# Performance work log

Hardware: AMD Instinct MI355X
Metric: run time of the kernel (lower is better)

## Reference

```python
import jax, jax.numpy as jnp
import numpy as np

N = 50000  # nodes


def gcn_layer(x, src, dst, W, b):
    """DGL GraphConv with norm='both': D_in^{-1/2} A^T D_out^{-1/2} x W + b."""
    E = src.shape[0]
    ones = jnp.ones((E,), dtype=x.dtype)
    deg_out = jax.ops.segment_sum(ones, src, num_segments=N)  # out-degree of src nodes
    deg_in = jax.ops.segment_sum(ones, dst, num_segments=N)   # in-degree of dst nodes
    norm_src = jax.lax.rsqrt(jnp.maximum(deg_out, 1.0))
    norm_dst = jax.lax.rsqrt(jnp.maximum(deg_in, 1.0))
    h = x * norm_src[:, None]
    agg = jax.ops.segment_sum(h[src], dst, num_segments=N)  # [N, in_dim]
    return (agg @ W) * norm_dst[:, None] + b


def encoder(feat, src, dst, W1, b1, W2, b2):
    h = jax.nn.relu(gcn_layer(feat, src, dst, W1, b1))
    h = jax.nn.relu(gcn_layer(h, src, dst, W2, b2))
    return h


def proj(h, fc1_W, fc1_b, fc2_W, fc2_b):
    z = jax.nn.elu(h @ fc1_W + fc1_b)
    return z @ fc2_W + fc2_b


def setup_inputs() -> dict:
    key = jax.random.key(0)
    ks = jax.random.split(key, 12)
    in_dim, hid, out_dim, E = 128, 128, 128, 800000
    inp = {
        "feat1": jax.random.normal(ks[0], (N, in_dim), dtype=jnp.float32),
        "feat2": jax.random.normal(ks[1], (N, in_dim), dtype=jnp.float32),
        "edge_index1": jax.random.randint(ks[2], (2, E), 0, N),
        "edge_index2": jax.random.randint(ks[3], (2, E), 0, N),
        # GraphConv weights: in_dim -> 2*hid -> hid
        "conv1_W": jax.random.normal(ks[4], (in_dim, 2 * hid), dtype=jnp.float32) * 0.05,
        "conv1_b": jnp.zeros((2 * hid,), dtype=jnp.float32),
        "conv2_W": jax.random.normal(ks[5], (2 * hid, hid), dtype=jnp.float32) * 0.05,
        "conv2_b": jnp.zeros((hid,), dtype=jnp.float32),
        # MLP proj: fc1 hid->out, fc2 out->hid
        "fc1_W": jax.random.normal(ks[6], (hid, out_dim), dtype=jnp.float32) * 0.05,
        "fc1_b": jnp.zeros((out_dim,), dtype=jnp.float32),
        "fc2_W": jax.random.normal(ks[7], (out_dim, hid), dtype=jnp.float32) * 0.05,
        "fc2_b": jnp.zeros((hid,), dtype=jnp.float32),
    }
    return inp


def reference(feat1, feat2, edge_index1, edge_index2,
              conv1_W, conv1_b, conv2_W, conv2_b,
              fc1_W, fc1_b, fc2_W, fc2_b):
    h1 = encoder(feat1, edge_index1[0], edge_index1[1], conv1_W, conv1_b, conv2_W, conv2_b)
    h2 = encoder(feat2, edge_index2[0], edge_index2[1], conv1_W, conv1_b, conv2_W, conv2_b)
    z1 = proj(h1, fc1_W, fc1_b, fc2_W, fc2_b)
    z2 = proj(h2, fc1_W, fc1_b, fc2_W, fc2_b)
    return (z1, z2)
```

## Files before the change

### kernel.cpp

```cpp
#include <hip/hip_runtime.h>
#include <math.h>

#define NDIM 128
#define H2   256
#define MAXG 2
#define TPE  8192
#define NBKMAX 512

typedef __attribute__((ext_vector_type(8))) short bf16x8;
typedef __attribute__((ext_vector_type(4))) float f32x4;

__device__ __forceinline__ unsigned short f2bf(float f) {
    unsigned int u = __float_as_uint(f);
    u += 0x7fffu + ((u >> 16) & 1u);
    return (unsigned short)(u >> 16);
}
__device__ __forceinline__ float bf2f(unsigned short h) {
    return __uint_as_float(((unsigned int)h) << 16);
}
__device__ __forceinline__ void split2(float f, unsigned short& h, unsigned short& l) {
    h = f2bf(f);
    l = f2bf(f - bf2f(h));
}

struct BinArgs {
    const int* src[MAXG]; const int* dst[MAXG];
    int* histD[MAXG]; int* histS[MAXG];
    int* totD[MAXG];  int* baseD[MAXG];
    int* totS[MAXG];  int* baseS[MAXG];
    unsigned int* pairs[MAXG];
    unsigned short* srcS[MAXG];
    int E[MAXG]; int NBK; int NT; int n;
};

__global__ __launch_bounds__(256) void binA(BinArgs a) {
    __shared__ int cntD[NBKMAX], cntS[NBKMAX];
    int g = blockIdx.y, t = blockIdx.x, tid = threadIdx.x;
    for (int b = tid; b < NBKMAX; b += 256) { cntD[b] = 0; cntS[b] = 0; }
    __syncthreads();
    int E = a.E[g];
    int base = t * TPE;
#pragma unroll
    for (int k = 0; k < TPE / 256; ++k) {
        int e = base + k * 256 + tid;
        if (e < E) {
            atomicAdd(&cntD[a.dst[g][e] >> 7], 1);
            atomicAdd(&cntS[a.src[g][e] >> 7], 1);
        }
    }
    __syncthreads();
    for (int b = tid; b < a.NBK; b += 256) {
        a.histD[g][t * a.NBK + b] = cntD[b];
        a.histS[g][t * a.NBK + b] = cntS[b];
    }
}

__global__ __launch_bounds__(512) void binB(BinArgs a) {
    int g = blockIdx.y, side = blockIdx.z;
    int* hist = side ? a.histS[g] : a.histD[g];
    int* tot  = side ? a.totS[g]  : a.totD[g];
    int* base = side ? a.baseS[g] : a.baseD[g];
    __shared__ int s[512];
    int b = threadIdx.x;
    int v = 0;
    if (b < a.NBK)
        for (int t = 0; t < a.NT; ++t) v += hist[t * a.NBK + b];
    s[b] = v;
    __syncthreads();
    for (int off = 1; off < 512; off <<= 1) {
        int u = (b >= off) ? s[b - off] : 0;
        __syncthreads();
        s[b] += u;
        __syncthreads();
    }
    int excl = s[b] - v;
    if (b < a.NBK) {
        tot[b] = v;
        base[b] = excl;
        int run = excl;
        for (int t = 0; t < a.NT; ++t) {
            int h = hist[t * a.NBK + b];
            hist[t * a.NBK + b] = run;
            run += h;
        }
    }
}

__global__ __launch_bounds__(256) void binC(BinArgs a) {
    __shared__ int offD[NBKMAX], offS[NBKMAX];
    int g = blockIdx.y, t = blockIdx.x, tid = threadIdx.x;
    for (int b = tid; b < a.NBK; b += 256) {
        offD[b] = a.histD[g][t * a.NBK + b];
        offS[b] = a.histS[g][t * a.NBK + b];
    }
    __syncthreads();
    int E = a.E[g];
    int base = t * TPE;
    unsigned int* pairs = a.pairs[g];
    unsigned short* ss = a.srcS[g];
#pragma unroll
    for (int k = 0; k < TPE / 256; ++k) {
        int e = base + k * 256 + tid;
        if (e < E) {
            int s = a.src[g][e], d = a.dst[g][e];
            int pos = atomicAdd(&offD[d >> 7], 1);
            pairs[pos] = ((unsigned int)(d & 127) << 16) | (unsigned int)s;
            int posS = atomicAdd(&offS[s >> 7], 1);
            ss[posS] = (unsigned short)s;
        }
    }
}

struct FinArgs {
    const unsigned int* pairs[MAXG];
    const unsigned short* srcS[MAXG];
    const int* totD[MAXG]; const int* baseD[MAXG];
    const int* totS[MAXG]; const int* baseS[MAXG];
    int* row_ptr[MAXG]; int* row_end[MAXG];
    unsigned short* edge_srt[MAXG];
    float* ns[MAXG]; float* nd[MAXG];
    int n;
};

__global__ __launch_bounds__(256) void finalize(FinArgs a) {
    __shared__ int cnt[128], hist[128], scn[128], cur[128];
    int g = blockIdx.y, bkt = blockIdx.x, tid = threadIdx.x;
    if (tid < 128) { cnt[tid] = 0; hist[tid] = 0; }
    __syncthreads();
    {
        int base = a.baseS[g][bkt], tot = a.totS[g][bkt];
        const unsigned short* ss = a.srcS[g];
        for (int i = tid; i < tot; i += 256)
            atomicAdd(&cnt[ss[base + i] & 127], 1);
    }
    int cntE = a.totD[g][bkt], base = a.baseD[g][bkt];
    const unsigned int* pp = a.pairs[g] + base;
    for (int i = tid; i < cntE; i += 256)
        atomicAdd(&hist[pp[i] >> 16], 1);
    __syncthreads();
    if (tid < 128) {
        int node = bkt * 128 + tid;
        if (node < a.n) {
            int c = cnt[tid];
            a.ns[g][node] = rsqrtf((float)(c > 1 ? c : 1));
        }
        scn[tid] = hist[tid];
    }
    __syncthreads();
    for (int off = 1; off < 128; off <<= 1) {
        int v = (tid < 128 && tid >= off) ? scn[tid - off] : 0;
        __syncthreads();
        if (tid < 128) scn[tid] += v;
        __syncthreads();
    }
    if (tid < 128) {
        int incl = scn[tid];
        int h = hist[tid];
        cur[tid] = incl - h;
        int node = bkt * 128 + tid;
        if (node < a.n) {
            a.row_ptr[g][node] = base + incl - h;
            a.row_end[g][node] = base + incl;
            a.nd[g][node] = rsqrtf((float)(h > 1 ? h : 1));
        }
    }
    __syncthreads();
    for (int i = tid; i < cntE; i += 256) {
        unsigned int p = pp[i];
        int pos = atomicAdd(&cur[p >> 16], 1);
        a.edge_srt[g][base + pos] = (unsigned short)(p & 0xFFFF);
    }
}

struct GatherArgs {
    const float* X[MAXG];
    const int* row_ptr[MAXG]; const int* row_end[MAXG];
    const unsigned short* edge_src[MAXG];
    const float* nd[MAXG];
    const float* sns[MAXG];
    unsigned short* outH[MAXG]; unsigned short* outL[MAXG];
    const float* bias; int use_nd; int use_sns; int n;
};

__global__ __launch_bounds__(256) void gather_split_b(GatherArgs a) {
    int g = blockIdx.y;
    int half = threadIdx.x >> 5;
    int lane = threadIdx.x & 31;
    int r = blockIdx.x * 8 + half;
    if (r >= a.n) return;
    int j = a.row_ptr[g][r];
    int end = a.row_end[g][r];
    const unsigned short* ep = a.edge_src[g];
    const float* X = a.X[g];
    const float* sns = a.sns[g];
    int base = lane * 4;
    float4 acc = make_float4(0.f, 0.f, 0.f, 0.f);
    if (a.use_sns) {
        for (; j + 3 < end; j += 4) {
            int s0 = ep[j], s1 = ep[j + 1], s2 = ep[j + 2], s3 = ep[j + 3];
            float n0 = sns[s0], n1 = sns[s1], n2 = sns[s2], n3 = sns[s3];
            float4 v0 = *(const float4*)(X + (size_t)s0 * NDIM + base);
            float4 v1 = *(const float4*)(X + (size_t)s1 * NDIM + base);
            float4 v2 = *(const float4*)(X + (size_t)s2 * NDIM + base);
            float4 v3 = *(const float4*)(X + (size_t)s3 * NDIM + base);
            acc.x = fmaf(v0.x, n0, fmaf(v1.x, n1, fmaf(v2.x, n2, fmaf(v3.x, n3, acc.x))));
            acc.y = fmaf(v0.y, n0, fmaf(v1.y, n1, fmaf(v2.y, n2, fmaf(v3.y, n3, acc.y))));
            acc.z = fmaf(v0.z, n0, fmaf(v1.z, n1, fmaf(v2.z, n2, fmaf(v3.z, n3, acc.z))));
            acc.w = fmaf(v0.w, n0, fmaf(v1.w, n1, fmaf(v2.w, n2, fmaf(v3.w, n3, acc.w))));
        }
        for (; j < end; ++j) {
            int s0 = ep[j];
            float n0 = sns[s0];
            float4 v0 = *(const float4*)(X + (size_t)s0 * NDIM + base);
            acc.x = fmaf(v0.x, n0, acc.x); acc.y = fmaf(v0.y, n0, acc.y);
            acc.z = fmaf(v0.z, n0, acc.z); acc.w = fmaf(v0.w, n0, acc.w);
        }
    } else {
        for (; j + 3 < end; j += 4) {
            int s0 = ep[j], s1 = ep[j + 1], s2 = ep[j + 2], s3 = ep[j + 3];
            float4 v0 = *(const float4*)(X + (size_t)s0 * NDIM + base);
            float4 v1 = *(const float4*)(X + (size_t)s1 * NDIM + base);
            float4 v2 = *(const float4*)(X + (size_t)s2 * NDIM + base);
            float4 v3 = *(const float4*)(X + (size_t)s3 * NDIM + base);
            acc.x += v0.x + v1.x + v2.x + v3.x;
            acc.y += v0.y + v1.y + v2.y + v3.y;
            acc.z += v0.z + v1.z + v2.z + v3.z;
            acc.w += v0.w + v1.w + v2.w + v3.w;
        }
        for (; j < end; ++j) {
            int s0 = ep[j];
            float4 v0 = *(const float4*)(X + (size_t)s0 * NDIM + base);
            acc.x += v0.x; acc.y += v0.y; acc.z += v0.z; acc.w += v0.w;
        }
    }
    float v[4] = {acc.x, acc.y, acc.z, acc.w};
    if (a.use_nd) {
        float s = a.nd[g][r];
#pragma unroll
        for (int i = 0; i < 4; ++i)
            v[i] = fmaxf(v[i] * s + a.bias[base + i], 0.f);
    }
    unsigned short h[4], l[4];
#pragma unroll
    for (int i = 0; i < 4; ++i) split2(v[i], h[i], l[i]);
    *(ushort4*)(a.outH[g] + (size_t)r * NDIM + base) = make_ushort4(h[0], h[1], h[2], h[3]);
    *(ushort4*)(a.outL[g] + (size_t)r * NDIM + base) = make_ushort4(l[0], l[1], l[2], l[3]);
}

__global__ void wprep_all(const float* __restrict__ W1, const float* __restrict__ W2,
                          const float* __restrict__ F1, const float* __restrict__ F2,
                          unsigned short* __restrict__ W1h, unsigned short* __restrict__ W1l,
                          unsigned short* __restrict__ W2h, unsigned short* __restrict__ W2l,
                          unsigned short* __restrict__ F1h, unsigned short* __restrict__ F1l,
                          unsigned short* __restrict__ F2h, unsigned short* __restrict__ F2l) {
    int i = blockIdx.x * 256 + threadIdx.x;
    const float* Wsrc; unsigned short *Hd, *Ld; int K, Nc, idx;
    if (i < 32768)       { Wsrc = W1; Hd = W1h; Ld = W1l; K = 128; Nc = 256; idx = i; }
    else if (i < 65536)  { Wsrc = W2; Hd = W2h; Ld = W2l; K = 256; Nc = 128; idx = i - 32768; }
    else if (i < 81920)  { Wsrc = F1; Hd = F1h; Ld = F1l; K = 128; Nc = 128; idx = i - 65536; }
    else                 { Wsrc = F2; Hd = F2h; Ld = F2l; K = 128; Nc = 128; idx = i - 81920; }
    int k = idx / Nc, n = idx % Nc;
    unsigned short h, l;
    split2(Wsrc[idx], h, l);
    Hd[n * K + k] = h;
    Ld[n * K + k] = l;
}

struct FusedArgs {
    const unsigned short* Ah[MAXG]; const unsigned short* Al[MAXG];
    const unsigned short* B1h; const unsigned short* B1l;
    const unsigned short* B2h; const unsigned short* B2l;
    const float* rs1[MAXG];
    const float* rs2[MAXG];
    const float* b1v;
    const float* b2v;
    float* C[MAXG];
    int M, has_rs1, has_rs2, has_b1, has_b2;
};

template <int K1, int N1, int ACT1, int ROWS>
__global__ __launch_bounds__(256) void fused_gemm2(FusedArgs a) {
    constexpr int IR  = ROWS / 16;
    constexpr int LDA = K1 + 8;
    constexpr int LDX = N1 + 8;
    constexpr int SH_A = ROWS * LDA;
    constexpr int SH_X = ROWS * LDX;
    constexpr int SH = (2 * SH_A > 2 * SH_X) ? 2 * SH_A : 2 * SH_X;
    __shared__ __align__(16) unsigned short S[SH];
    unsigned short* As_h = S;
    unsigned short* As_l = S + SH_A;
    unsigned short* Xs_h = S;
    unsigned short* Xs_l = S + SH_X;

    int g = blockIdx.y;
    const unsigned short* __restrict__ Ah_g = a.Ah[g];
    const unsigned short* __restrict__ Al_g = a.Al[g];

    int tid  = threadIdx.x;
    int wave = tid >> 6, lane = tid & 63;
    int quad = lane >> 4, l16 = lane & 15;
    int rowBase = blockIdx.x * ROWS;
    int M = a.M;

    constexpr int CPR = K1 / 8;
#pragma unroll
    for (int c0 = 0; c0 < ROWS * CPR; c0 += 256) {
        int c = c0 + tid;
        int row = c / CPR;
        int col = (c % CPR) * 8;
        int gr = rowBase + row;
        uint4 vh = make_uint4(0, 0, 0, 0), vl = make_uint4(0, 0, 0, 0);
        if (gr < M) {
            vh = *(const uint4*)(Ah_g + (size_t)gr * K1 + col);
            vl = *(const uint4*)(Al_g + (size_t)gr * K1 + col);
        }
        *(uint4*)(As_h + row * LDA + col) = vh;
        *(uint4*)(As_l + row * LDA + col) = vl;
    }
    __syncthreads();

    constexpr int J1 = N1 / 64;
    int wcol1 = wave * (N1 / 4);
    f32x4 acc1[IR][J1] = {};
#pragma unroll
    for (int kt = 0; kt < K1 / 32; ++kt) {
        int kc = kt * 32 + quad * 8;
        bf16x8 af[IR], alf[IR];
#pragma unroll
        for (int i = 0; i < IR; ++i) {
            af[i]  = *(const bf16x8*)(As_h + (i * 16 + l16) * LDA + kc);
            alf[i] = *(const bf16x8*)(As_l + (i * 16 + l16) * LDA + kc);
        }
        bf16x8 bh_[J1], bl_[J1];
#pragma unroll
        for (int j = 0; j < J1; ++j) {
            size_t bo = (size_t)(wcol1 + j * 16 + l16) * K1 + kt * 32 + quad * 8;
            bh_[j] = *(const bf16x8*)(a.B1h + bo);
            bl_[j] = *(const bf16x8*)(a.B1l + bo);
        }
#pragma unroll
        for (int i = 0; i < IR; ++i)
#pragma unroll
            for (int j = 0; j < J1; ++j) {
                acc1[i][j] = __builtin_amdgcn_mfma_f32_16x16x32_bf16(af[i],  bh_[j], acc1[i][j], 0, 0, 0);
                acc1[i][j] = __builtin_amdgcn_mfma_f32_16x16x32_bf16(alf[i], bh_[j], acc1[i][j], 0, 0, 0);
                acc1[i][j] = __builtin_amdgcn_mfma_f32_16x16x32_bf16(af[i],  bl_[j], acc1[i][j], 0, 0, 0);
            }
    }
    __syncthreads();

    const float* rs1p = a.has_rs1 ? a.rs1[g] : nullptr;
#pragma unroll
    for (int i = 0; i < IR; ++i) {
#pragma unroll
        for (int r = 0; r < 4; ++r) {
            int row  = i * 16 + quad * 4 + r;
            int grow = rowBase + row;
            float rs = 1.0f;
            if (rs1p) rs = (grow < M) ? rs1p[grow] : 0.0f;
#pragma unroll
            for (int j = 0; j < J1; ++j) {
                int col = wcol1 + j * 16 + l16;
                float v = acc1[i][j][r] * rs;
                if (a.has_b1) v += a.b1v[col];
                if (ACT1 == 1) v = fmaxf(v, 0.f);
                else           v = v > 0.f ? v : expm1f(v);
                unsigned short h, l;
                split2(v, h, l);
                Xs_h[row * LDX + col] = h;
                Xs_l[row * LDX + col] = l;
            }
        }
    }
    __syncthreads();

    int wcol2 = wave * 32;
    f32x4 acc2[IR][2] = {};
#pragma unroll
    for (int kt = 0; kt < N1 / 32; ++kt) {
        int kc = kt * 32 + quad * 8;
        bf16x8 xf[IR], xlf[IR];
#pragma unroll
        for (int i = 0; i < IR; ++i) {
            xf[i]  = *(const bf16x8*)(Xs_h + (i * 16 + l16) * LDX + kc);
            xlf[i] = *(const bf16x8*)(Xs_l + (i * 16 + l16) * LDX + kc);
        }
        bf16x8 bh_[2], bl_[2];
#pragma unroll
        for (int j = 0; j < 2; ++j) {
            size_t bo = (size_t)(wcol2 + j * 16 + l16) * N1 + kt * 32 + quad * 8;
            bh_[j] = *(const bf16x8*)(a.B2h + bo);
            bl_[j] = *(const bf16x8*)(a.B2l + bo);
        }
#pragma unroll
        for (int i = 0; i < IR; ++i)
#pragma unroll
            for (int j = 0; j < 2; ++j) {
                acc2[i][j] = __builtin_amdgcn_mfma_f32_16x16x32_bf16(xf[i],  bh_[j], acc2[i][j], 0, 0, 0);
                acc2[i][j] = __builtin_amdgcn_mfma_f32_16x16x32_bf16(xlf[i], bh_[j], acc2[i][j], 0, 0, 0);
                acc2[i][j] = __builtin_amdgcn_mfma_f32_16x16x32_bf16(xf[i],  bl_[j], acc2[i][j], 0, 0, 0);
            }
    }

    const float* rs2p = a.has_rs2 ? a.rs2[g] : nullptr;
#pragma unroll
    for (int i = 0; i < IR; ++i) {
#pragma unroll
        for (int r = 0; r < 4; ++r) {
            int grow = rowBase + i * 16 + quad * 4 + r;
            if (grow >= M) continue;
            float rs = rs2p ? rs2p[grow] : 1.0f;
#pragma unroll
            for (int j = 0; j < 2; ++j) {
                int col = wcol2 + j * 16 + l16;
                float v = acc2[i][j][r] * rs;
                if (a.has_b2) v += a.b2v[col];
                a.C[g][(size_t)grow * NDIM + col] = v;
            }
        }
    }
}

extern "C" void kernel_launch(void* const* d_in, const int* in_sizes, int n_in,
                              void* d_out, int out_size, void* d_ws, size_t ws_size,
                              hipStream_t stream) {
    const float* feat[2] = {(const float*)d_in[0], (const float*)d_in[1]};
    const int*   ei[2]   = {(const int*)d_in[2], (const int*)d_in[3]};
    const float* W1   = (const float*)d_in[4];
    const float* b1   = (const float*)d_in[5];
    const float* W2   = (const float*)d_in[6];
    const float* b2   = (const float*)d_in[7];
    const float* fc1W = (const float*)d_in[8];
    const float* fc1b = (const float*)d_in[9];
    const float* fc2W = (const float*)d_in[10];
    const float* fc2b = (const float*)d_in[11];
    int N = in_sizes[0] / NDIM;
    float* out = (float*)d_out;

    int Emax = 0;
    for (int g = 0; g < 2; ++g) { int E = in_sizes[2 + g] / 2; if (E > Emax) Emax = E; }
    int NBK = (N + 127) / 128;
    int NT  = (Emax + TPE - 1) / TPE;

    char* p = (char*)d_ws;
    float* ns_[2]; float* nd_[2];
    for (int i = 0; i < 2; ++i) { ns_[i] = (float*)p; p += (size_t)N * 4; }
    for (int i = 0; i < 2; ++i) { nd_[i] = (float*)p; p += (size_t)N * 4; }
    int* rp_[2]; int* re_[2]; unsigned short* esrt_[2];
    for (int i = 0; i < 2; ++i) { rp_[i] = (int*)p; p += (size_t)N * 4; }
    for (int i = 0; i < 2; ++i) { re_[i] = (int*)p; p += (size_t)N * 4; }
    for (int i = 0; i < 2; ++i) { esrt_[i] = (unsigned short*)p; p += (size_t)Emax * 2; }
    unsigned short* R1[2]; unsigned short* R2[2];
    for (int i = 0; i < 2; ++i) { R1[i] = (unsigned short*)p; p += (size_t)N * NDIM * 2 * 2; }
    for (int i = 0; i < 2; ++i) { R2[i] = (unsigned short*)p; p += (size_t)N * H2 * 2 * 2; }
    unsigned short* W1th = (unsigned short*)p; p += (size_t)NDIM * H2 * 2;
    unsigned short* W1tl = (unsigned short*)p; p += (size_t)NDIM * H2 * 2;
    unsigned short* W2th = (unsigned short*)p; p += (size_t)H2 * NDIM * 2;
    unsigned short* W2tl = (unsigned short*)p; p += (size_t)H2 * NDIM * 2;
    unsigned short* f1th = (unsigned short*)p; p += (size_t)NDIM * NDIM * 2;
    unsigned short* f1tl = (unsigned short*)p; p += (size_t)NDIM * NDIM * 2;
    unsigned short* f2th = (unsigned short*)p; p += (size_t)NDIM * NDIM * 2;
    unsigned short* f2tl = (unsigned short*)p; p += (size_t)NDIM * NDIM * 2;
    int* tb = (int*)p; p += (size_t)2 * 4 * NBK * 4;

    int* histD_[2]; int* histS_[2]; unsigned int* pairs_[2]; unsigned short* srcS_[2];
    for (int i = 0; i < 2; ++i) {
        histD_[i] = (int*)R2[i];
        histS_[i] = (int*)R2[i] + (size_t)NT * NBK;
        pairs_[i] = (unsigned int*)((char*)R2[i] + (1 << 20));
        srcS_[i]  = (unsigned short*)R1[i];
    }

    BinArgs ba = {};
    ba.NBK = NBK; ba.NT = NT; ba.n = N;
    for (int i = 0; i < 2; ++i) {
        int E = in_sizes[2 + i] / 2;
        ba.src[i] = ei[i]; ba.dst[i] = ei[i] + E; ba.E[i] = E;
        ba.histD[i] = histD_[i]; ba.histS[i] = histS_[i];
        ba.totD[i]  = tb + (size_t)i * 4 * NBK;
        ba.baseD[i] = tb + (size_t)i * 4 * NBK + NBK;
        ba.totS[i]  = tb + (size_t)i * 4 * NBK + 2 * NBK;
        ba.baseS[i] = tb + (size_t)i * 4 * NBK + 3 * NBK;
        ba.pairs[i] = pairs_[i]; ba.srcS[i] = srcS_[i];
    }

    wprep_all<<<384, 256, 0, stream>>>(W1, W2, fc1W, fc2W,
                                       W1th, W1tl, W2th, W2tl, f1th, f1tl, f2th, f2tl);
    binA<<<dim3(NT, 2), 256, 0, stream>>>(ba);
    binB<<<dim3(1, 2, 2), 512, 0, stream>>>(ba);
    binC<<<dim3(NT, 2), 256, 0, stream>>>(ba);

    FinArgs fa = {};
    fa.n = N;
    for (int i = 0; i < 2; ++i) {
        fa.pairs[i] = pairs_[i]; fa.srcS[i] = srcS_[i];
        fa.totD[i] = ba.totD[i]; fa.baseD[i] = ba.baseD[i];
        fa.totS[i] = ba.totS[i]; fa.baseS[i] = ba.baseS[i];
        fa.row_ptr[i] = rp_[i]; fa.row_end[i] = re_[i];
        fa.edge_srt[i] = esrt_[i];
        fa.ns[i] = ns_[i]; fa.nd[i] = nd_[i];
    }
    finalize<<<dim3(NBK, 2), 256, 0, stream>>>(fa);

    unsigned short *A1h[2], *A1l[2], *Gh[2], *Gl[2];
    float* T[2];
    for (int i = 0; i < 2; ++i) {
        A1h[i] = R1[i]; A1l[i] = R1[i] + (size_t)N * NDIM;
        T[i]   = (float*)R2[i];
        Gh[i]  = R2[i] + (size_t)N * 256;
        Gl[i]  = R2[i] + (size_t)N * 256 + (size_t)N * NDIM;
    }

    int ggrid = (N + 7) / 8;
    int mgrid32 = (N + 31) / 32;

    GatherArgs ga = {};
    ga.n = N; ga.use_nd = 0; ga.use_sns = 1; ga.bias = b2;
    for (int i = 0; i < 2; ++i) {
        ga.X[i] = feat[i];
        ga.row_ptr[i] = rp_[i]; ga.row_end[i] = re_[i]; ga.edge_src[i] = esrt_[i];
        ga.nd[i] = nd_[i]; ga.sns[i] = ns_[i];
        ga.outH[i] = A1h[i]; ga.outL[i] = A1l[i];
    }
    gather_split_b<<<dim3(ggrid, 2), 256, 0, stream>>>(ga);

    FusedArgs f12 = {};
    f12.B1h = W1th; f12.B1l = W1tl; f12.B2h = W2th; f12.B2l = W2tl;
    f12.b1v = b1; f12.has_b1 = 1; f12.has_b2 = 0;
    f12.has_rs1 = 1; f12.has_rs2 = 1;
    f12.M = N;
    for (int i = 0; i < 2; ++i) {
        f12.Ah[i] = A1h[i]; f12.Al[i] = A1l[i];
        f12.rs1[i] = nd_[i]; f12.rs2[i] = ns_[i];
        f12.C[i] = T[i];
    }
    fused_gemm2<128, 256, 1, 32><<<dim3(mgrid32, 2), 256, 0, stream>>>(f12);

    GatherArgs gb = ga;
    gb.use_nd = 1; gb.use_sns = 0;
    for (int i = 0; i < 2; ++i) {
        gb.X[i] = T[i];
        gb.outH[i] = Gh[i]; gb.outL[i] = Gl[i];
    }
    gather_split_b<<<dim3(ggrid, 2), 256, 0, stream>>>(gb);

    FusedArgs f34 = {};
    f34.B1h = f1th; f34.B1l = f1tl; f34.B2h = f2th; f34.B2l = f2tl;
    f34.b1v = fc1b; f34.has_b1 = 1; f34.b2v = fc2b; f34.has_b2 = 1;
    f34.has_rs1 = 0; f34.has_rs2 = 0;
    f34.M = N;
    for (int i = 0; i < 2; ++i) {
        f34.Ah[i] = Gh[i]; f34.Al[i] = Gl[i];
        f34.C[i] = out + (size_t)i * N * NDIM;
    }
    fused_gemm2<128, 128, 2, 32><<<dim3(mgrid32, 2), 256, 0, stream>>>(f34);
}
```

Measured before the change: 613.6 us.

## Overlap gather and GEMM stages across graphs with interleaved fat kernels

Instead of processing both graphs in each stage together, the stages are software-pipelined across the two graphs. Each launch co-schedules the GEMM blocks for one graph with the gather blocks for the other, interleaving them by block index inside a single kernel. The aim is to overlap the memory-latency-bound gather with the compute-bound MFMA GEMM and so raise device utilisation. In exchange the fat kernel always reserves the GEMM's shared memory, which can lower occupancy for the gather blocks, and there are now five launches instead of four.

```diff
diff --git a/kernel.cpp b/kernel.cpp
--- a/kernel.cpp
+++ b/kernel.cpp
@@ -172,27 +172,37 @@
     }
 }
 
-struct GatherArgs {
-    const float* X[MAXG];
-    const int* row_ptr[MAXG]; const int* row_end[MAXG];
-    const unsigned short* edge_src[MAXG];
-    const float* nd[MAXG];
-    const float* sns[MAXG];
-    unsigned short* outH[MAXG]; unsigned short* outL[MAXG];
-    const float* bias; int use_nd; int use_sns; int n;
+struct GatherP {
+    const float* X;
+    const int* row_ptr; const int* row_end;
+    const unsigned short* edge_src;
+    const float* nd; const float* sns;
+    unsigned short* outH; unsigned short* outL;
+    const float* bias; int use_nd, use_sns, n;
 };
 
-__global__ __launch_bounds__(256) void gather_split_b(GatherArgs a) {
-    int g = blockIdx.y;
+struct FusedP {
+    const unsigned short* Ah; const unsigned short* Al;
+    const unsigned short* B1h; const unsigned short* B1l;
+    const unsigned short* B2h; const unsigned short* B2l;
+    const float* rs1; const float* rs2;
+    const float* b1v; const float* b2v;
+    float* C;
+    int M, has_rs1, has_rs2, has_b1, has_b2;
+};
+
+struct FatP { FusedP m; GatherP g; int nM, nG; };
+
+__device__ __forceinline__ void gather_body(const GatherP& a, int bx) {
     int half = threadIdx.x >> 5;
     int lane = threadIdx.x & 31;
-    int r = blockIdx.x * 8 + half;
+    int r = bx * 8 + half;
     if (r >= a.n) return;
-    int j = a.row_ptr[g][r];
-    int end = a.row_end[g][r];
-    const unsigned short* ep = a.edge_src[g];
-    const float* X = a.X[g];
-    const float* sns = a.sns[g];
+    int j = a.row_ptr[r];
+    int end = a.row_end[r];
+    const unsigned short* ep = a.edge_src;
+    const float* X = a.X;
+    const float* sns = a.sns;
     int base = lane * 4;
     float4 acc = make_float4(0.f, 0.f, 0.f, 0.f);
     if (a.use_sns) {
@@ -235,7 +245,7 @@
     }
     float v[4] = {acc.x, acc.y, acc.z, acc.w};
     if (a.use_nd) {
-        float s = a.nd[g][r];
+        float s = a.nd[r];
 #pragma unroll
         for (int i = 0; i < 4; ++i)
             v[i] = fmaxf(v[i] * s + a.bias[base + i], 0.f);
@@ -243,8 +253,8 @@
     unsigned short h[4], l[4];
 #pragma unroll
     for (int i = 0; i < 4; ++i) split2(v[i], h[i], l[i]);
-    *(ushort4*)(a.outH[g] + (size_t)r * NDIM + base) = make_ushort4(h[0], h[1], h[2], h[3]);
-    *(ushort4*)(a.outL[g] + (size_t)r * NDIM + base) = make_ushort4(l[0], l[1], l[2], l[3]);
+    *(ushort4*)(a.outH + (size_t)r * NDIM + base) = make_ushort4(h[0], h[1], h[2], h[3]);
+    *(ushort4*)(a.outL + (size_t)r * NDIM + base) = make_ushort4(l[0], l[1], l[2], l[3]);
 }
 
 __global__ void wprep_all(const float* __restrict__ W1, const float* __restrict__ W2,
@@ -266,40 +276,25 @@
     Ld[n * K + k] = l;
 }
 
-struct FusedArgs {
-    const unsigned short* Ah[MAXG]; const unsigned short* Al[MAXG];
-    const unsigned short* B1h; const unsigned short* B1l;
-    const unsigned short* B2h; const unsigned short* B2l;
-    const float* rs1[MAXG];
-    const float* rs2[MAXG];
-    const float* b1v;
-    const float* b2v;
-    float* C[MAXG];
-    int M, has_rs1, has_rs2, has_b1, has_b2;
-};
-
 template <int K1, int N1, int ACT1, int ROWS>
-__global__ __launch_bounds__(256) void fused_gemm2(FusedArgs a) {
+__device__ __forceinline__ void gemm_body(const FusedP& a, int bx, unsigned short* S) {
     constexpr int IR  = ROWS / 16;
     constexpr int LDA = K1 + 8;
     constexpr int LDX = N1 + 8;
     constexpr int SH_A = ROWS * LDA;
     constexpr int SH_X = ROWS * LDX;
-    constexpr int SH = (2 * SH_A > 2 * SH_X) ? 2 * SH_A : 2 * SH_X;
-    __shared__ __align__(16) unsigned short S[SH];
     unsigned short* As_h = S;
     unsigned short* As_l = S + SH_A;
     unsigned short* Xs_h = S;
     unsigned short* Xs_l = S + SH_X;
 
-    int g = blockIdx.y;
-    const unsigned short* __restrict__ Ah_g = a.Ah[g];
-    const unsigned short* __restrict__ Al_g = a.Al[g];
+    const unsigned short* __restrict__ Ah_g = a.Ah;
+    const unsigned short* __restrict__ Al_g = a.Al;
 
     int tid  = threadIdx.x;
     int wave = tid >> 6, lane = tid & 63;
     int quad = lane >> 4, l16 = lane & 15;
-    int rowBase = blockIdx.x * ROWS;
+    int rowBase = bx * ROWS;
     int M = a.M;
 
     constexpr int CPR = K1 / 8;
@@ -349,7 +344,7 @@
     }
     __syncthreads();
 
-    const float* rs1p = a.has_rs1 ? a.rs1[g] : nullptr;
+    const float* rs1p = a.has_rs1 ? a.rs1 : nullptr;
 #pragma unroll
     for (int i = 0; i < IR; ++i) {
 #pragma unroll
@@ -402,7 +397,7 @@
             }
     }
 
-    const float* rs2p = a.has_rs2 ? a.rs2[g] : nullptr;
+    const float* rs2p = a.has_rs2 ? a.rs2 : nullptr;
 #pragma unroll
     for (int i = 0; i < IR; ++i) {
 #pragma unroll
@@ -415,10 +410,47 @@
                 int col = wcol2 + j * 16 + l16;
                 float v = acc2[i][j][r] * rs;
                 if (a.has_b2) v += a.b2v[col];
-                a.C[g][(size_t)grow * NDIM + col] = v;
+                a.C[(size_t)grow * NDIM + col] = v;
             }
         }
     }
+}
+
+template <int K1, int N1, int ROWS>
+constexpr int sh_shorts() {
+    int A = 2 * ROWS * (K1 + 8);
+    int X = 2 * ROWS * (N1 + 8);
+    return A > X ? A : X;
+}
+
+__global__ __launch_bounds__(256) void gather_one(GatherP a) { gather_body(a, blockIdx.x); }
+
+template <int K1, int N1, int ACT1, int ROWS>
+__global__ __launch_bounds__(256) void fused_one(FusedP a) {
+    __shared__ __align__(16) unsigned short S[sh_shorts<K1, N1, ROWS>()];
+    gemm_body<K1, N1, ACT1, ROWS>(a, blockIdx.x, S);
+}
+
+template <int K1, int N1, int ACT1, int ROWS>
+__global__ __launch_bounds__(256) void fat_k(FatP a) {
+    __shared__ __align__(16) unsigned short S[sh_shorts<K1, N1, ROWS>()];
+    int bid = blockIdx.x;
+    bool isGemm;
+    int mIdx = 0, gIdx = 0;
+    if (a.nM == 0)      { isGemm = false; gIdx = bid; }
+    else if (a.nG == 0) { isGemm = true;  mIdx = bid; }
+    else {
+        int R = (a.nM + a.nG) / a.nM; if (R < 1) R = 1;
+        int q = bid / R, r = bid % R;
+        if (r == 0 && q < a.nM) { isGemm = true; mIdx = q; }
+        else {
+            isGemm = false;
+            int c = (r == 0) ? a.nM : ((q + 1 < a.nM) ? (q + 1) : a.nM);
+            gIdx = bid - c;
+        }
+    }
+    if (isGemm) gemm_body<K1, N1, ACT1, ROWS>(a.m, mIdx, S);
+    else        gather_body(a.g, gIdx);
 }
 
 extern "C" void kernel_launch(void* const* d_in, const int* in_sizes, int n_in,
@@ -514,44 +546,45 @@
     int ggrid = (N + 7) / 8;
     int mgrid32 = (N + 31) / 32;
 
-    GatherArgs ga = {};
-    ga.n = N; ga.use_nd = 0; ga.use_sns = 1; ga.bias = b2;
+    GatherP ga1[2], ga2[2];
+    FusedP f12[2], f34[2];
     for (int i = 0; i < 2; ++i) {
-        ga.X[i] = feat[i];
-        ga.row_ptr[i] = rp_[i]; ga.row_end[i] = re_[i]; ga.edge_src[i] = esrt_[i];
-        ga.nd[i] = nd_[i]; ga.sns[i] = ns_[i];
-        ga.outH[i] = A1h[i]; ga.outL[i] = A1l[i];
-    }
-    gather_split_b<<<dim3(ggrid, 2), 256, 0, stream>>>(ga);
-
-    FusedArgs f12 = {};
-    f12.B1h = W1th; f12.B1l = W1tl; f12.B2h = W2th; f12.B2l = W2tl;
-    f12.b1v = b1; f12.has_b1 = 1; f12.has_b2 = 0;
-    f12.has_rs1 = 1; f12.has_rs2 = 1;
-    f12.M = N;
-    for (int i = 0; i < 2; ++i) {
-        f12.Ah[i] = A1h[i]; f12.Al[i] = A1l[i];
-        f12.rs1[i] = nd_[i]; f12.rs2[i] = ns_[i];
-        f12.C[i] = T[i];
-    }
-    fused_gemm2<128, 256, 1, 32><<<dim3(mgrid32, 2), 256, 0, stream>>>(f12);
-
-    GatherArgs gb = ga;
-    gb.use_nd = 1; gb.use_sns = 0;
-    for (int i = 0; i < 2; ++i) {
-        gb.X[i] = T[i];
-        gb.outH[i] = Gh[i]; gb.outL[i] = Gl[i];
-    }
-    gather_split_b<<<dim3(ggrid, 2), 256, 0, stream>>>(gb);
-
-    FusedArgs f34 = {};
-    f34.B1h = f1th; f34.B1l = f1tl; f34.B2h = f2th; f34.B2l = f2tl;
-    f34.b1v = fc1b; f34.has_b1 = 1; f34.b2v = fc2b; f34.has_b2 = 1;
-    f34.has_rs1 = 0; f34.has_rs2 = 0;
-    f34.M = N;
-    for (int i = 0; i < 2; ++i) {
-        f34.Ah[i] = Gh[i]; f34.Al[i] = Gl[i];
-        f34.C[i] = out + (size_t)i * N * NDIM;
-    }
-    fused_gemm2<128, 128, 2, 32><<<dim3(mgrid32, 2), 256, 0, stream>>>(f34);
-}
+        ga1[i] = {};
+        ga1[i].X = feat[i];
+        ga1[i].row_ptr = rp_[i]; ga1[i].row_end = re_[i]; ga1[i].edge_src = esrt_[i];
+        ga1[i].nd = nd_[i]; ga1[i].sns = ns_[i];
+        ga1[i].outH = A1h[i]; ga1[i].outL = A1l[i];
+        ga1[i].bias = b2; ga1[i].use_nd = 0; ga1[i].use_sns = 1; ga1[i].n = N;
+        ga2[i] = ga1[i];
+        ga2[i].X = T[i]; ga2[i].use_nd = 1; ga2[i].use_sns = 0;
+        ga2[i].outH = Gh[i]; ga2[i].outL = Gl[i];
+        f12[i] = {};
+        f12[i].Ah = A1h[i]; f12[i].Al = A1l[i];
+        f12[i].B1h = W1th; f12[i].B1l = W1tl; f12[i].B2h = W2th; f12[i].B2l = W2tl;
+        f12[i].rs1 = nd_[i]; f12[i].rs2 = ns_[i];
+        f12[i].b1v = b1;
+        f12[i].C = T[i];
+        f12[i].M = N; f12[i].has_rs1 = 1; f12[i].has_rs2 = 1; f12[i].has_b1 = 1; f12[i].has_b2 = 0;
+        f34[i] = {};
+        f34[i].Ah = Gh[i]; f34[i].Al = Gl[i];
+        f34[i].B1h = f1th; f34[i].B1l = f1tl; f34[i].B2h = f2th; f34[i].B2l = f2tl;
+        f34[i].b1v = fc1b; f34[i].b2v = fc2b;
+        f34[i].C = out + (size_t)i * N * NDIM;
+        f34[i].M = N; f34[i].has_rs1 = 0; f34[i].has_rs2 = 0; f34[i].has_b1 = 1; f34[i].has_b2 = 1;
+    }
+
+    gather_one<<<ggrid, 256, 0, stream>>>(ga1[0]);
+    {
+        FatP fp = {f12[0], ga1[1], mgrid32, ggrid};
+        fat_k<128, 256, 1, 32><<<mgrid32 + ggrid, 256, 0, stream>>>(fp);
+    }
+    {
+        FatP fp = {f12[1], ga2[0], mgrid32, ggrid};
+        fat_k<128, 256, 1, 32><<<mgrid32 + ggrid, 256, 0, stream>>>(fp);
+    }
+    {
+        FatP fp = {f34[0], ga2[1], mgrid32, ggrid};
+        fat_k<128, 128, 2, 32><<<mgrid32 + ggrid, 256, 0, stream>>>(fp);
+    }
+    fused_one<128, 128, 2, 32><<<mgrid32, 256, 0, stream>>>(f34[1]);
+}
```

Result: slower. 885.2 us (+44.2%).

## Double-buffer global B-fragment loads and raise fused GEMM tile to 64 rows

Applied to the files above, without the earlier changes.

The fused two-GEMM kernel now prefetches the next k-step's weight fragments from global memory into alternating register buffers while MFMAs run on the current ones. The first B tiles are issued before the A-tile staging into shared memory, so their latency overlaps that copy. Rows per block go from 32 to 64, which halves the grid and doubles how many times each weight fragment is reused per block. The cost is higher register and LDS pressure per block, which may lower occupancy, and fewer blocks across the device.

```diff
diff --git a/kernel.cpp b/kernel.cpp
--- a/kernel.cpp
+++ b/kernel.cpp
@@ -295,12 +295,49 @@
     int g = blockIdx.y;
     const unsigned short* __restrict__ Ah_g = a.Ah[g];
     const unsigned short* __restrict__ Al_g = a.Al[g];
+    const unsigned short* __restrict__ B1h = a.B1h;
+    const unsigned short* __restrict__ B1l = a.B1l;
+    const unsigned short* __restrict__ B2h = a.B2h;
+    const unsigned short* __restrict__ B2l = a.B2l;
 
     int tid  = threadIdx.x;
     int wave = tid >> 6, lane = tid & 63;
     int quad = lane >> 4, l16 = lane & 15;
     int rowBase = blockIdx.x * ROWS;
     int M = a.M;
+
+    constexpr int J1  = N1 / 64;
+    constexpr int KT1 = K1 / 32;
+    constexpr int KT2 = N1 / 32;
+    int wcol1 = wave * (N1 / 4);
+    int wcol2 = wave * 32;
+
+    size_t b1off[J1];
+#pragma unroll
+    for (int j = 0; j < J1; ++j)
+        b1off[j] = (size_t)(wcol1 + j * 16 + l16) * K1 + quad * 8;
+    size_t b2off[2];
+#pragma unroll
+    for (int j = 0; j < 2; ++j)
+        b2off[j] = (size_t)(wcol2 + j * 16 + l16) * N1 + quad * 8;
+
+    auto loadB1 = [&](int kt, bf16x8 (&bh)[J1], bf16x8 (&bl)[J1]) {
+#pragma unroll
+        for (int j = 0; j < J1; ++j) {
+            bh[j] = *(const bf16x8*)(B1h + b1off[j] + kt * 32);
+            bl[j] = *(const bf16x8*)(B1l + b1off[j] + kt * 32);
+        }
+    };
+    auto loadB2 = [&](int kt, bf16x8 (&bh)[2], bf16x8 (&bl)[2]) {
+#pragma unroll
+        for (int j = 0; j < 2; ++j) {
+            bh[j] = *(const bf16x8*)(B2h + b2off[j] + kt * 32);
+            bl[j] = *(const bf16x8*)(B2l + b2off[j] + kt * 32);
+        }
+    };
+
+    bf16x8 b1hA[J1], b1lA[J1], b1hB[J1], b1lB[J1];
+    loadB1(0, b1hA, b1lA);
 
     constexpr int CPR = K1 / 8;
 #pragma unroll
@@ -319,11 +356,8 @@
     }
     __syncthreads();
 
-    constexpr int J1 = N1 / 64;
-    int wcol1 = wave * (N1 / 4);
     f32x4 acc1[IR][J1] = {};
-#pragma unroll
-    for (int kt = 0; kt < K1 / 32; ++kt) {
+    auto stepP1 = [&](int kt, bf16x8 (&bh)[J1], bf16x8 (&bl)[J1]) {
         int kc = kt * 32 + quad * 8;
         bf16x8 af[IR], alf[IR];
 #pragma unroll
@@ -331,22 +365,26 @@
             af[i]  = *(const bf16x8*)(As_h + (i * 16 + l16) * LDA + kc);
             alf[i] = *(const bf16x8*)(As_l + (i * 16 + l16) * LDA + kc);
         }
-        bf16x8 bh_[J1], bl_[J1];
-#pragma unroll
-        for (int j = 0; j < J1; ++j) {
-            size_t bo = (size_t)(wcol1 + j * 16 + l16) * K1 + kt * 32 + quad * 8;
-            bh_[j] = *(const bf16x8*)(a.B1h + bo);
-            bl_[j] = *(const bf16x8*)(a.B1l + bo);
-        }
 #pragma unroll
         for (int i = 0; i < IR; ++i)
 #pragma unroll
             for (int j = 0; j < J1; ++j) {
-                acc1[i][j] = __builtin_amdgcn_mfma_f32_16x16x32_bf16(af[i],  bh_[j], acc1[i][j], 0, 0, 0);
-                acc1[i][j] = __builtin_amdgcn_mfma_f32_16x16x32_bf16(alf[i], bh_[j], acc1[i][j], 0, 0, 0);
-                acc1[i][j] = __builtin_amdgcn_mfma_f32_16x16x32_bf16(af[i],  bl_[j], acc1[i][j], 0, 0, 0);
+                acc1[i][j] = __builtin_amdgcn_mfma_f32_16x16x32_bf16(af[i],  bh[j], acc1[i][j], 0, 0, 0);
+                acc1[i][j] = __builtin_amdgcn_mfma_f32_16x16x32_bf16(alf[i], bh[j], acc1[i][j], 0, 0, 0);
+                acc1[i][j] = __builtin_amdgcn_mfma_f32_16x16x32_bf16(af[i],  bl[j], acc1[i][j], 0, 0, 0);
             }
-    }
+    };
+#pragma unroll
+    for (int kt = 0; kt < KT1; kt += 2) {
+        if (kt + 1 < KT1) loadB1(kt + 1, b1hB, b1lB);
+        stepP1(kt, b1hA, b1lA);
+        if (kt + 2 < KT1) loadB1(kt + 2, b1hA, b1lA);
+        if (kt + 1 < KT1) stepP1(kt + 1, b1hB, b1lB);
+    }
+
+    bf16x8 b2hA[2], b2lA[2], b2hB[2], b2lB[2];
+    loadB2(0, b2hA, b2lA);
+
     __syncthreads();
 
     const float* rs1p = a.has_rs1 ? a.rs1[g] : nullptr;
@@ -374,10 +412,8 @@
     }
     __syncthreads();
 
-    int wcol2 = wave * 32;
     f32x4 acc2[IR][2] = {};
-#pragma unroll
-    for (int kt = 0; kt < N1 / 32; ++kt) {
+    auto stepP2 = [&](int kt, bf16x8 (&bh)[2], bf16x8 (&bl)[2]) {
         int kc = kt * 32 + quad * 8;
         bf16x8 xf[IR], xlf[IR];
 #pragma unroll
@@ -385,21 +421,21 @@
             xf[i]  = *(const bf16x8*)(Xs_h + (i * 16 + l16) * LDX + kc);
             xlf[i] = *(const bf16x8*)(Xs_l + (i * 16 + l16) * LDX + kc);
         }
-        bf16x8 bh_[2], bl_[2];
-#pragma unroll
-        for (int j = 0; j < 2; ++j) {
-            size_t bo = (size_t)(wcol2 + j * 16 + l16) * N1 + kt * 32 + quad * 8;
-            bh_[j] = *(const bf16x8*)(a.B2h + bo);
-            bl_[j] = *(const bf16x8*)(a.B2l + bo);
-        }
 #pragma unroll
         for (int i = 0; i < IR; ++i)
 #pragma unroll
             for (int j = 0; j < 2; ++j) {
-                acc2[i][j] = __builtin_amdgcn_mfma_f32_16x16x32_bf16(xf[i],  bh_[j], acc2[i][j], 0, 0, 0);
-                acc2[i][j] = __builtin_amdgcn_mfma_f32_16x16x32_bf16(xlf[i], bh_[j], acc2[i][j], 0, 0, 0);
-                acc2[i][j] = __builtin_amdgcn_mfma_f32_16x16x32_bf16(xf[i],  bl_[j], acc2[i][j], 0, 0, 0);
+                acc2[i][j] = __builtin_amdgcn_mfma_f32_16x16x32_bf16(xf[i],  bh[j], acc2[i][j], 0, 0, 0);
+                acc2[i][j] = __builtin_amdgcn_mfma_f32_16x16x32_bf16(xlf[i], bh[j], acc2[i][j], 0, 0, 0);
+                acc2[i][j] = __builtin_amdgcn_mfma_f32_16x16x32_bf16(xf[i],  bl[j], acc2[i][j], 0, 0, 0);
             }
+    };
+#pragma unroll
+    for (int kt = 0; kt < KT2; kt += 2) {
+        if (kt + 1 < KT2) loadB2(kt + 1, b2hB, b2lB);
+        stepP2(kt, b2hA, b2lA);
+        if (kt + 2 < KT2) loadB2(kt + 2, b2hA, b2lA);
+        if (kt + 1 < KT2) stepP2(kt + 1, b2hB, b2lB);
     }
 
     const float* rs2p = a.has_rs2 ? a.rs2[g] : nullptr;
@@ -512,7 +548,7 @@
     }
 
     int ggrid = (N + 7) / 8;
-    int mgrid32 = (N + 31) / 32;
+    int mgrid = (N + 63) / 64;
 
     GatherArgs ga = {};
     ga.n = N; ga.use_nd = 0; ga.use_sns = 1; ga.bias = b2;
@@ -534,7 +570,7 @@
         f12.rs1[i] = nd_[i]; f12.rs2[i] = ns_[i];
         f12.C[i] = T[i];
     }
-    fused_gemm2<128, 256, 1, 32><<<dim3(mgrid32, 2), 256, 0, stream>>>(f12);
+    fused_gemm2<128, 256, 1, 64><<<dim3(mgrid, 2), 256, 0, stream>>>(f12);
 
     GatherArgs gb = ga;
     gb.use_nd = 1; gb.use_sns = 0;
@@ -553,5 +589,5 @@
         f34.Ah[i] = Gh[i]; f34.Al[i] = Gl[i];
         f34.C[i] = out + (size_t)i * N * NDIM;
     }
-    fused_gemm2<128, 128, 2, 32><<<dim3(mgrid32, 2), 256, 0, stream>>>(f34);
-}
+    fused_gemm2<128, 128, 2, 64><<<dim3(mgrid, 2), 256, 0, stream>>>(f34);
+}
```

Measured after the change: 593.3 us. 1.03x faster.
